# Optimization experiments

Hardware: AMD Instinct MI355X
Metric: run time of the kernel (lower is better)

The kernel has to match this reference:

```python
import jax, jax.numpy as jnp
import numpy as np

N = 100_000   # nodes
E = 1_600_000 # edges (avg degree 16)
B = 512       # graphs in batch
F_IN = 64; H = 4; D = 64; HD = H * D; EXTRA = 16
NEG_SLOPE = 0.2  # DGL GATConv default


def _gat_conv(x, src, dst, W, al, ar, bias):
    """DGL GATConv: fc -> per-head attn logits -> edge leaky_relu -> segment softmax over dst -> scatter-sum."""
    h = (x @ W).reshape(N, H, D)                       # [N,H,D]
    el = jnp.sum(h * al, axis=-1)                      # [N,H]
    er = jnp.sum(h * ar, axis=-1)                      # [N,H]
    e = jax.nn.leaky_relu(el[src] + er[dst], NEG_SLOPE)  # [E,H]
    m = jax.ops.segment_max(e, dst, num_segments=N)    # [N,H]
    m = jnp.where(jnp.isfinite(m), m, 0.0)             # guard empty segments
    ex = jnp.exp(e - m[dst])                           # [E,H]
    den = jax.ops.segment_sum(ex, dst, num_segments=N) # [N,H]
    alpha = ex / jnp.maximum(den[dst], 1e-9)           # [E,H]
    msg = h[src] * alpha[:, :, None]                   # [E,H,D]
    out = jax.ops.segment_sum(msg, dst, num_segments=N) + bias.reshape(1, H, D)
    return out  # [N,H,D]


def setup_inputs() -> dict:
    key = jax.random.key(0)
    ks = jax.random.split(key, 26)
    nrm = lambda k, shape: jax.random.normal(k, shape, dtype=jnp.float32) * 0.5
    src = jax.random.randint(ks[0], (E,), 0, N)
    # ensure every node has >=1 incoming edge (DGL disallows zero in-degree by default)
    dst = jnp.concatenate([jnp.arange(N), jax.random.randint(ks[1], (E - N,), 0, N)])
    node_graph = jnp.sort(jax.random.randint(ks[2], (N,), 0, B))
    inp = dict(
        src=src, dst=dst, node_graph=node_graph,
        feats_node=jax.random.normal(ks[3], (N, F_IN), dtype=jnp.float32),
        feats_graph=jax.random.normal(ks[4], (B, EXTRA), dtype=jnp.float32),
        W1=nrm(ks[5], (F_IN, HD)), al1=nrm(ks[6], (H, D)), ar1=nrm(ks[7], (H, D)), bg1=jnp.zeros(HD),
        W2=nrm(ks[8], (HD, HD)),  al2=nrm(ks[9], (H, D)), ar2=nrm(ks[10], (H, D)), bg2=jnp.zeros(HD),
        W3=nrm(ks[11], (HD, HD)), al3=nrm(ks[12], (H, D)), ar3=nrm(ks[13], (H, D)), bg3=jnp.zeros(HD),
        sw=nrm(ks[14], (HD, 1)), sb=jnp.zeros(1),
        lw1=nrm(ks[15], (HD + EXTRA, 2 * D)), lb1=jnp.zeros(2 * D),
        lw2=nrm(ks[16], (2 * D, D)), lb2=jnp.zeros(D),
        lw3=nrm(ks[17], (D, 1)), lb3=jnp.zeros(1),
    )
    return inp


def reference(src, dst, node_graph, feats_node, feats_graph,
              W1, al1, ar1, bg1, W2, al2, ar2, bg2, W3, al3, ar3, bg3,
              sw, sb, lw1, lb1, lw2, lb2, lw3, lb3):
    selu = jax.nn.selu
    x = selu(_gat_conv(feats_node, src, dst, W1, al1, ar1, bg1)).reshape(N, HD)
    x = selu(_gat_conv(x, src, dst, W2, al2, ar2, bg2)).reshape(N, HD)
    x = selu(_gat_conv(x, src, dst, W3, al3, ar3, bg3)).reshape(N, HD)
    # WeightedAverage readout: sigmoid-scored weighted mean per graph
    w = jax.nn.sigmoid(x @ sw + sb)                               # [N,1]
    num = jax.ops.segment_sum(w * x, node_graph, num_segments=B)  # [B,HD]
    den = jax.ops.segment_sum(w, node_graph, num_segments=B)      # [B,1]
    emb = num / jnp.maximum(den, 1e-9)
    y = jnp.concatenate([emb, feats_graph], axis=1)
    y = selu(y @ lw1 + lb1)
    y = selu(y @ lw2 + lb2)
    return y @ lw3 + lb3  # [B,1]
```

## Files before the change

kernel.cpp:

```cpp
#include <hip/hip_runtime.h>

#define N_NODES 100000
#define N_EDGES 1600000
#define N_GRAPHS 512
#define F_IN 64
#define HD 256
#define EXTRA 16
#define SCAN_BLOCK 512

typedef float f32x4 __attribute__((ext_vector_type(4)));
typedef _Float16 f16x4 __attribute__((ext_vector_type(4)));
typedef _Float16 f16x8 __attribute__((ext_vector_type(8)));

__device__ __forceinline__ float selu_f(float x) {
    const float a = 1.6732632423543772f, sc = 1.0507009873554805f;
    return x > 0.f ? sc * x : sc * a * (__expf(x) - 1.f);
}

__global__ __launch_bounds__(256) void hist_k(const int* __restrict__ dst, int* __restrict__ hist) {
    int j = blockIdx.x * 256 + threadIdx.x;
    if (j < N_EDGES) atomicAdd(&hist[dst[j]], 1);
}

__global__ __launch_bounds__(SCAN_BLOCK) void scan1_k(const int* __restrict__ hist,
                                                      int* __restrict__ row_ptr,
                                                      int* __restrict__ bsums) {
    __shared__ int sm[SCAN_BLOCK];
    int t = threadIdx.x;
    int i = blockIdx.x * SCAN_BLOCK + t;
    int v = (i < N_NODES) ? hist[i] : 0;
    sm[t] = v;
    __syncthreads();
    for (int off = 1; off < SCAN_BLOCK; off <<= 1) {
        int add = (t >= off) ? sm[t - off] : 0;
        __syncthreads();
        sm[t] += add;
        __syncthreads();
    }
    if (i < N_NODES) row_ptr[i] = sm[t] - v;
    if (t == SCAN_BLOCK - 1) bsums[blockIdx.x] = sm[t];
}

__global__ __launch_bounds__(256) void scan2_k(int* __restrict__ bsums, int nb) {
    __shared__ int sm[256];
    int t = threadIdx.x;
    int v = (t < nb) ? bsums[t] : 0;
    sm[t] = v;
    __syncthreads();
    for (int off = 1; off < 256; off <<= 1) {
        int add = (t >= off) ? sm[t - off] : 0;
        __syncthreads();
        sm[t] += add;
        __syncthreads();
    }
    if (t < nb) bsums[t] = sm[t] - v;
}

__global__ __launch_bounds__(256) void scan3_k(int* __restrict__ row_ptr, const int* __restrict__ bsums) {
    int i = blockIdx.x * 256 + threadIdx.x;
    if (i < N_NODES) row_ptr[i] += bsums[i / SCAN_BLOCK];
    if (i == 0) row_ptr[N_NODES] = N_EDGES;
}

__global__ __launch_bounds__(256) void scatter_k(const int* __restrict__ src,
                                                 const int* __restrict__ dst,
                                                 const int* __restrict__ row_ptr,
                                                 int* __restrict__ cursor,
                                                 int* __restrict__ csr_src) {
    int j = blockIdx.x * 256 + threadIdx.x;
    if (j < N_EDGES) {
        int d = dst[j];
        int r = atomicAdd(&cursor[d], 1);
        csr_src[row_ptr[d] + r] = src[j];
    }
}

__global__ __launch_bounds__(256) void gbound_k(const int* __restrict__ node_graph, int* __restrict__ gstart) {
    int g = blockIdx.x * 256 + threadIdx.x;
    if (g > N_GRAPHS) return;
    int lo = 0, hi = N_NODES;
    while (lo < hi) {
        int mid = (lo + hi) >> 1;
        if (node_graph[mid] < g) lo = mid + 1; else hi = mid;
    }
    gstart[g] = lo;
}

__global__ __launch_bounds__(256) void tcast_split_k(const float* __restrict__ W,
                                                     _Float16* __restrict__ Wt_hi,
                                                     _Float16* __restrict__ Wt_lo, int K) {
    int idx = blockIdx.x * 256 + threadIdx.x;
    if (idx >= K * HD) return;
    int n = idx / K, k = idx - n * K;
    float w = W[(size_t)k * HD + n];
    _Float16 hi = (_Float16)w;
    _Float16 lo = (_Float16)(w - (float)hi);
    Wt_hi[idx] = hi;
    Wt_lo[idx] = lo;
}

template <int K>
__global__ __launch_bounds__(256) void gemm_split_k(const float* __restrict__ A,
                                                    const _Float16* __restrict__ Bt_hi,
                                                    const _Float16* __restrict__ Bt_lo,
                                                    const float* __restrict__ al,
                                                    const float* __restrict__ ar,
                                                    _Float16* __restrict__ Chi,
                                                    float* __restrict__ el,
                                                    float* __restrict__ er, int M) {
    const int BM = 128, BN = 128, LDP = 40;
    __shared__ _Float16 As_hi[BM][LDP];
    __shared__ _Float16 As_lo[BM][LDP];
    __shared__ _Float16 Bs_hi[BN][LDP];
    __shared__ _Float16 Bs_lo[BN][LDP];
    int tid = threadIdx.x;
    int wave = tid >> 6, lane = tid & 63;
    int q = lane >> 4, l16 = lane & 15;
    int row0 = blockIdx.y * BM, col0 = blockIdx.x * BN;
    f32x4 acc[2][8] = {};

    for (int k0 = 0; k0 < K; k0 += 32) {
#pragma unroll
        for (int c = 0; c < 4; c++) {
            int cc = tid + c * 256;
            int r = cc >> 3, o = (cc & 7) * 4;
            int gr = row0 + r;
            float4 v = make_float4(0.f, 0.f, 0.f, 0.f);
            if (gr < M) v = *(const float4*)(A + (size_t)gr * K + k0 + o);
            f16x4 hi, lo;
            hi.x = (_Float16)v.x; lo.x = (_Float16)(v.x - (float)hi.x);
            hi.y = (_Float16)v.y; lo.y = (_Float16)(v.y - (float)hi.y);
            hi.z = (_Float16)v.z; lo.z = (_Float16)(v.z - (float)hi.z);
            hi.w = (_Float16)v.w; lo.w = (_Float16)(v.w - (float)hi.w);
            *(f16x4*)&As_hi[r][o] = hi;
            *(f16x4*)&As_lo[r][o] = lo;
        }
#pragma unroll
        for (int c = 0; c < 2; c++) {
            int cc = tid + c * 256;
            int n = cc >> 2, o = (cc & 3) * 8;
            *(f16x8*)&Bs_hi[n][o] = *(const f16x8*)(Bt_hi + (size_t)(col0 + n) * K + k0 + o);
            *(f16x8*)&Bs_lo[n][o] = *(const f16x8*)(Bt_lo + (size_t)(col0 + n) * K + k0 + o);
        }
        __syncthreads();

        f16x8 ah[2], alo2[2];
#pragma unroll
        for (int ms = 0; ms < 2; ms++) {
            int m = wave * 32 + ms * 16 + l16;
            ah[ms] = *(const f16x8*)&As_hi[m][q * 8];
            alo2[ms] = *(const f16x8*)&As_lo[m][q * 8];
        }
#pragma unroll
        for (int ns = 0; ns < 8; ns++) {
            int n = ns * 16 + l16;
            f16x8 bh = *(const f16x8*)&Bs_hi[n][q * 8];
            f16x8 bl = *(const f16x8*)&Bs_lo[n][q * 8];
#pragma unroll
            for (int ms = 0; ms < 2; ms++) {
                acc[ms][ns] = __builtin_amdgcn_mfma_f32_16x16x32_f16(ah[ms], bh, acc[ms][ns], 0, 0, 0);
                acc[ms][ns] = __builtin_amdgcn_mfma_f32_16x16x32_f16(ah[ms], bl, acc[ms][ns], 0, 0, 0);
                acc[ms][ns] = __builtin_amdgcn_mfma_f32_16x16x32_f16(alo2[ms], bh, acc[ms][ns], 0, 0, 0);
            }
        }
        __syncthreads();
    }

    const int h0 = col0 >> 6;
    float alv[8], arv[8];
#pragma unroll
    for (int ns = 0; ns < 8; ns++) {
        int hh = h0 + (ns >> 2);
        int d = (ns & 3) * 16 + l16;
        alv[ns] = al[hh * 64 + d];
        arv[ns] = ar[hh * 64 + d];
    }
#pragma unroll
    for (int ms = 0; ms < 2; ms++) {
#pragma unroll
        for (int i = 0; i < 4; i++) {
            int r = row0 + wave * 32 + ms * 16 + q * 4 + i;
            bool ok = r < M;
            float el0 = 0.f, er0 = 0.f, el1 = 0.f, er1 = 0.f;
#pragma unroll
            for (int ns = 0; ns < 8; ns++) {
                float v = acc[ms][ns][i];
                if (ok) Chi[(size_t)r * HD + col0 + ns * 16 + l16] = (_Float16)v;
                if (ns < 4) { el0 = fmaf(v, alv[ns], el0); er0 = fmaf(v, arv[ns], er0); }
                else        { el1 = fmaf(v, alv[ns], el1); er1 = fmaf(v, arv[ns], er1); }
            }
#pragma unroll
            for (int off = 1; off < 16; off <<= 1) {
                el0 += __shfl_xor(el0, off, 64);
                er0 += __shfl_xor(er0, off, 64);
                el1 += __shfl_xor(el1, off, 64);
                er1 += __shfl_xor(er1, off, 64);
            }
            if (l16 == 0 && ok) {
                el[(size_t)r * 4 + h0] = el0;
                el[(size_t)r * 4 + h0 + 1] = el1;
                er[(size_t)r * 4 + h0] = er0;
                er[(size_t)r * 4 + h0 + 1] = er1;
            }
        }
    }
}

__global__ __launch_bounds__(256) void gat_aggregate_k(const _Float16* __restrict__ hb,
                                                       const float* __restrict__ el,
                                                       const float* __restrict__ er,
                                                       const int* __restrict__ csr_src,
                                                       const int* __restrict__ row_ptr,
                                                       const float* __restrict__ bias,
                                                       float* __restrict__ xout) {
    __shared__ float wlds[4][64][4];
    __shared__ int snlds[4][64];
    int wv = threadIdx.x >> 6;
    int lane = threadIdx.x & 63;
    int v = blockIdx.x * 4 + wv;
    bool valid = v < N_NODES;
    int vc = valid ? v : 0;
    int rs = row_ptr[vc];
    int deg = valid ? row_ptr[vc + 1] - rs : 0;
    float4 erv = make_float4(0.f, 0.f, 0.f, 0.f);
    if (valid) erv = *(const float4*)(er + (size_t)vc * 4);

    float m[4] = {-1e30f, -1e30f, -1e30f, -1e30f};
    float s[4] = {0.f, 0.f, 0.f, 0.f};
    float m_h = 0.f, inv_den = 1.f, er_h = 0.f;
    int head = lane >> 4;

    if (deg <= 64) {
        int my_sn = 0;
        float my_e[4] = {0.f, 0.f, 0.f, 0.f};
        if (lane < deg) {
            int sn = csr_src[rs + lane];
            my_sn = sn;
            float4 elv = *(const float4*)(el + (size_t)sn * 4);
            float e0 = elv.x + erv.x, e1 = elv.y + erv.y, e2 = elv.z + erv.z, e3 = elv.w + erv.w;
            my_e[0] = e0 > 0.f ? e0 : 0.2f * e0;
            my_e[1] = e1 > 0.f ? e1 : 0.2f * e1;
            my_e[2] = e2 > 0.f ? e2 : 0.2f * e2;
            my_e[3] = e3 > 0.f ? e3 : 0.2f * e3;
#pragma unroll
            for (int hh = 0; hh < 4; hh++) { m[hh] = my_e[hh]; s[hh] = 1.f; }
        }
        for (int off = 1; off < deg && off < 64; off <<= 1) {
#pragma unroll
            for (int hh = 0; hh < 4; hh++) {
                float mo = __shfl_xor(m[hh], off, 64);
                float so = __shfl_xor(s[hh], off, 64);
                float mn = fmaxf(m[hh], mo);
                s[hh] = s[hh] * __expf(m[hh] - mn) + so * __expf(mo - mn);
                m[hh] = mn;
            }
        }
        if (lane < deg) {
#pragma unroll
            for (int hh = 0; hh < 4; hh++)
                wlds[wv][lane][hh] = __expf(my_e[hh] - m[hh]) / fmaxf(s[hh], 1e-9f);
            snlds[wv][lane] = my_sn;
        }
    } else {
        for (int t = lane; t < deg; t += 64) {
            int sn = csr_src[rs + t];
            float4 elv = *(const float4*)(el + (size_t)sn * 4);
            float e[4];
            e[0] = elv.x + erv.x; e[1] = elv.y + erv.y; e[2] = elv.z + erv.z; e[3] = elv.w + erv.w;
#pragma unroll
            for (int hh = 0; hh < 4; hh++) {
                float ev = e[hh] > 0.f ? e[hh] : 0.2f * e[hh];
                float mn = fmaxf(m[hh], ev);
                s[hh] = s[hh] * __expf(m[hh] - mn) + __expf(ev - mn);
                m[hh] = mn;
            }
        }
#pragma unroll
        for (int off = 32; off >= 1; off >>= 1) {
#pragma unroll
            for (int hh = 0; hh < 4; hh++) {
                float mo = __shfl_xor(m[hh], off, 64);
                float so = __shfl_xor(s[hh], off, 64);
                float mn = fmaxf(m[hh], mo);
                s[hh] = s[hh] * __expf(m[hh] - mn) + so * __expf(mo - mn);
                m[hh] = mn;
            }
        }
        m_h = head == 0 ? m[0] : head == 1 ? m[1] : head == 2 ? m[2] : m[3];
        float den = head == 0 ? s[0] : head == 1 ? s[1] : head == 2 ? s[2] : s[3];
        er_h = head == 0 ? erv.x : head == 1 ? erv.y : head == 2 ? erv.z : erv.w;
        inv_den = 1.f / fmaxf(den, 1e-9f);
    }
    __syncthreads();

    float a0 = 0.f, a1 = 0.f, a2 = 0.f, a3 = 0.f;
    if (deg <= 64) {
        int t = 0;
        for (; t + 8 <= deg; t += 8) {
            int sn[8];
            float w[8];
#pragma unroll
            for (int u = 0; u < 8; u++) {
                sn[u] = snlds[wv][t + u];
                w[u] = wlds[wv][t + u][head];
            }
            f16x4 hv[8];
#pragma unroll
            for (int u = 0; u < 8; u++)
                hv[u] = *(const f16x4*)(hb + (size_t)sn[u] * HD + lane * 4);
#pragma unroll
            for (int u = 0; u < 8; u++) {
                a0 = fmaf(w[u], (float)hv[u].x, a0);
                a1 = fmaf(w[u], (float)hv[u].y, a1);
                a2 = fmaf(w[u], (float)hv[u].z, a2);
                a3 = fmaf(w[u], (float)hv[u].w, a3);
            }
        }
        for (; t < deg; t++) {
            int sn = snlds[wv][t];
            float w = wlds[wv][t][head];
            f16x4 hv = *(const f16x4*)(hb + (size_t)sn * HD + lane * 4);
            a0 = fmaf(w, (float)hv.x, a0);
            a1 = fmaf(w, (float)hv.y, a1);
            a2 = fmaf(w, (float)hv.z, a2);
            a3 = fmaf(w, (float)hv.w, a3);
        }
    } else {
        for (int t = 0; t < deg; t++) {
            int sn = csr_src[rs + t];
            float e = el[(size_t)sn * 4 + head] + er_h;
            e = e > 0.f ? e : 0.2f * e;
            float w = __expf(e - m_h) * inv_den;
            f16x4 hv = *(const f16x4*)(hb + (size_t)sn * HD + lane * 4);
            a0 = fmaf(w, (float)hv.x, a0);
            a1 = fmaf(w, (float)hv.y, a1);
            a2 = fmaf(w, (float)hv.z, a2);
            a3 = fmaf(w, (float)hv.w, a3);
        }
    }
    if (valid) {
        float4 bv = *(const float4*)(bias + lane * 4);
        float4 o;
        o.x = selu_f(a0 + bv.x);
        o.y = selu_f(a1 + bv.y);
        o.z = selu_f(a2 + bv.z);
        o.w = selu_f(a3 + bv.w);
        *(float4*)(xout + (size_t)v * HD + lane * 4) = o;
    }
}

__global__ __launch_bounds__(256) void score_k(const float* __restrict__ x,
                                               const float* __restrict__ sw,
                                               const float* __restrict__ sb,
                                               float* __restrict__ wsc) {
    int n = (blockIdx.x * 256 + threadIdx.x) / 64;
    int lane = threadIdx.x & 63;
    if (n >= N_NODES) return;
    float4 xv = *(const float4*)(x + (size_t)n * HD + lane * 4);
    float4 sv = *(const float4*)(sw + lane * 4);
    float p = xv.x * sv.x + xv.y * sv.y + xv.z * sv.z + xv.w * sv.w;
#pragma unroll
    for (int off = 1; off < 64; off <<= 1) p += __shfl_xor(p, off, 64);
    if (lane == 0) wsc[n] = 1.f / (1.f + __expf(-(p + sb[0])));
}

__global__ __launch_bounds__(256) void readout_k(const float* __restrict__ x,
                                                 const float* __restrict__ wsc,
                                                 const int* __restrict__ gstart,
                                                 const float* __restrict__ fg,
                                                 float* __restrict__ y0) {
    int g = blockIdx.x;
    int f = threadIdx.x;
    int s = gstart[g], e = gstart[g + 1];
    float num = 0.f, den = 0.f;
    for (int n = s; n < e; n++) {
        float wn = wsc[n];
        num = fmaf(wn, x[(size_t)n * HD + f], num);
        den += wn;
    }
    float emb = num / fmaxf(den, 1e-9f);
    y0[(size_t)g * 272 + f] = emb;
    if (f < EXTRA) y0[(size_t)g * 272 + 256 + f] = fg[g * EXTRA + f];
}

__global__ __launch_bounds__(128) void mlp_k(const float* __restrict__ y0g,
                                             const float* __restrict__ lw1, const float* __restrict__ lb1,
                                             const float* __restrict__ lw2, const float* __restrict__ lb2,
                                             const float* __restrict__ lw3, const float* __restrict__ lb3,
                                             float* __restrict__ out) {
    __shared__ float y0s[272];
    __shared__ float y1s[128];
    int g = blockIdx.x, t = threadIdx.x;
    for (int i = t; i < 272; i += 128) y0s[i] = y0g[(size_t)g * 272 + i];
    __syncthreads();
    float acc = lb1[t];
    for (int k = 0; k < 272; k++) acc = fmaf(y0s[k], lw1[k * 128 + t], acc);
    y1s[t] = selu_f(acc);
    __syncthreads();
    if (t < 64) {
        float a2 = lb2[t];
        for (int k = 0; k < 128; k++) a2 = fmaf(y1s[k], lw2[k * 64 + t], a2);
        float v2 = selu_f(a2);
        float p = v2 * lw3[t];
#pragma unroll
        for (int off = 1; off < 64; off <<= 1) p += __shfl_xor(p, off, 64);
        if (t == 0) out[g] = p + lb3[0];
    }
}

extern "C" void kernel_launch(void* const* d_in, const int* in_sizes, int n_in,
                              void* d_out, int out_size, void* d_ws, size_t ws_size,
                              hipStream_t stream) {
    const int* src = (const int*)d_in[0];
    const int* dst = (const int*)d_in[1];
    const int* node_graph = (const int*)d_in[2];
    const float* feats_node = (const float*)d_in[3];
    const float* feats_graph = (const float*)d_in[4];
    const float* W1 = (const float*)d_in[5];
    const float* al1 = (const float*)d_in[6];
    const float* ar1 = (const float*)d_in[7];
    const float* bg1 = (const float*)d_in[8];
    const float* W2 = (const float*)d_in[9];
    const float* al2 = (const float*)d_in[10];
    const float* ar2 = (const float*)d_in[11];
    const float* bg2 = (const float*)d_in[12];
    const float* W3 = (const float*)d_in[13];
    const float* al3 = (const float*)d_in[14];
    const float* ar3 = (const float*)d_in[15];
    const float* bg3 = (const float*)d_in[16];
    const float* sw = (const float*)d_in[17];
    const float* sb = (const float*)d_in[18];
    const float* lw1 = (const float*)d_in[19];
    const float* lb1 = (const float*)d_in[20];
    const float* lw2 = (const float*)d_in[21];
    const float* lb2 = (const float*)d_in[22];
    const float* lw3 = (const float*)d_in[23];
    const float* lb3 = (const float*)d_in[24];
    float* out = (float*)d_out;

    char* ws = (char*)d_ws;
    size_t off = 0;
    auto alloc = [&](size_t bytes) -> char* {
        char* p = ws + off;
        off += (bytes + 255) & ~(size_t)255;
        return p;
    };
    float* xf32 = (float*)alloc((size_t)N_NODES * HD * 4);
    _Float16* hhi = (_Float16*)alloc((size_t)N_NODES * HD * 2);
    _Float16* W1hi = (_Float16*)alloc((size_t)F_IN * HD * 2);
    _Float16* W1lo = (_Float16*)alloc((size_t)F_IN * HD * 2);
    _Float16* W2hi = (_Float16*)alloc((size_t)HD * HD * 2);
    _Float16* W2lo = (_Float16*)alloc((size_t)HD * HD * 2);
    _Float16* W3hi = (_Float16*)alloc((size_t)HD * HD * 2);
    _Float16* W3lo = (_Float16*)alloc((size_t)HD * HD * 2);
    float* el = (float*)alloc((size_t)N_NODES * 4 * 4);
    float* er = (float*)alloc((size_t)N_NODES * 4 * 4);
    float* wsc = (float*)alloc((size_t)N_NODES * 4);
    float* y0 = (float*)alloc((size_t)N_GRAPHS * 272 * 4);
    int* hist = (int*)alloc((size_t)N_NODES * 4);
    int* row_ptr = (int*)alloc((size_t)(N_NODES + 1) * 4);
    int* cursor = (int*)alloc((size_t)N_NODES * 4);
    int* csr_src = (int*)alloc((size_t)N_EDGES * 4);
    int* gstart = (int*)alloc((size_t)(N_GRAPHS + 1) * 4);
    int* bsums = (int*)alloc(256 * 4);
    (void)ws_size; (void)in_sizes; (void)n_in; (void)out_size;

    hipMemsetAsync(hist, 0, (size_t)N_NODES * 4, stream);
    hipMemsetAsync(cursor, 0, (size_t)N_NODES * 4, stream);

    hist_k<<<(N_EDGES + 255) / 256, 256, 0, stream>>>(dst, hist);
    int nb = (N_NODES + SCAN_BLOCK - 1) / SCAN_BLOCK;
    scan1_k<<<nb, SCAN_BLOCK, 0, stream>>>(hist, row_ptr, bsums);
    scan2_k<<<1, 256, 0, stream>>>(bsums, nb);
    scan3_k<<<(N_NODES + 255) / 256, 256, 0, stream>>>(row_ptr, bsums);
    scatter_k<<<(N_EDGES + 255) / 256, 256, 0, stream>>>(src, dst, row_ptr, cursor, csr_src);
    gbound_k<<<3, 256, 0, stream>>>(node_graph, gstart);

    tcast_split_k<<<(F_IN * HD + 255) / 256, 256, 0, stream>>>(W1, W1hi, W1lo, F_IN);
    tcast_split_k<<<(HD * HD + 255) / 256, 256, 0, stream>>>(W2, W2hi, W2lo, HD);
    tcast_split_k<<<(HD * HD + 255) / 256, 256, 0, stream>>>(W3, W3hi, W3lo, HD);

    dim3 ggrid(HD / 128, (N_NODES + 127) / 128);
    int nwb = (N_NODES + 3) / 4;

    gemm_split_k<F_IN><<<ggrid, 256, 0, stream>>>(feats_node, W1hi, W1lo, al1, ar1, hhi, el, er, N_NODES);
    gat_aggregate_k<<<nwb, 256, 0, stream>>>(hhi, el, er, csr_src, row_ptr, bg1, xf32);
    gemm_split_k<HD><<<ggrid, 256, 0, stream>>>(xf32, W2hi, W2lo, al2, ar2, hhi, el, er, N_NODES);
    gat_aggregate_k<<<nwb, 256, 0, stream>>>(hhi, el, er, csr_src, row_ptr, bg2, xf32);
    gemm_split_k<HD><<<ggrid, 256, 0, stream>>>(xf32, W3hi, W3lo, al3, ar3, hhi, el, er, N_NODES);
    gat_aggregate_k<<<nwb, 256, 0, stream>>>(hhi, el, er, csr_src, row_ptr, bg3, xf32);

    score_k<<<nwb, 256, 0, stream>>>(xf32, sw, sb, wsc);
    readout_k<<<N_GRAPHS, 256, 0, stream>>>(xf32, wsc, gstart, feats_graph, y0);
    mlp_k<<<N_GRAPHS, 128, 0, stream>>>(y0, lw1, lb1, lw2, lb2, lw3, lb3, out);
}
```

Baseline: 1.012 ms.

## Fuse readout scoring into last aggregate and defer softmax normalization

The sigmoid score computation moves into the final GAT aggregation kernel via a template flag, which removes the separate score kernel and its re-read of the node feature matrix. The small-degree softmax switches from an online max/sum shuffle merge to a separate max pass followed by a sum pass. Normalization by the denominator is applied once at the output instead of per edge weight. The readout loop also gets an unroll hint. The risk is small extra register pressure in the aggregate kernel and a slightly different floating-point ordering.

```diff
diff --git a/kernel.cpp b/kernel.cpp
--- a/kernel.cpp
+++ b/kernel.cpp
@@ -206,13 +206,17 @@
     }
 }
 
+template <int OUT>
 __global__ __launch_bounds__(256) void gat_aggregate_k(const _Float16* __restrict__ hb,
                                                        const float* __restrict__ el,
                                                        const float* __restrict__ er,
                                                        const int* __restrict__ csr_src,
                                                        const int* __restrict__ row_ptr,
                                                        const float* __restrict__ bias,
-                                                       float* __restrict__ xout) {
+                                                       float* __restrict__ xout,
+                                                       const float* __restrict__ sw,
+                                                       const float* __restrict__ sb,
+                                                       float* __restrict__ wsc) {
     __shared__ float wlds[4][64][4];
     __shared__ int snlds[4][64];
     int wv = threadIdx.x >> 6;
@@ -225,43 +229,55 @@
     float4 erv = make_float4(0.f, 0.f, 0.f, 0.f);
     if (valid) erv = *(const float4*)(er + (size_t)vc * 4);
 
-    float m[4] = {-1e30f, -1e30f, -1e30f, -1e30f};
-    float s[4] = {0.f, 0.f, 0.f, 0.f};
-    float m_h = 0.f, inv_den = 1.f, er_h = 0.f;
     int head = lane >> 4;
+    float inv_den = 1.f;
+    float m_h = 0.f, er_h = 0.f;
 
     if (deg <= 64) {
+        float e0 = -1e30f, e1 = -1e30f, e2 = -1e30f, e3 = -1e30f;
         int my_sn = 0;
-        float my_e[4] = {0.f, 0.f, 0.f, 0.f};
         if (lane < deg) {
-            int sn = csr_src[rs + lane];
-            my_sn = sn;
-            float4 elv = *(const float4*)(el + (size_t)sn * 4);
-            float e0 = elv.x + erv.x, e1 = elv.y + erv.y, e2 = elv.z + erv.z, e3 = elv.w + erv.w;
-            my_e[0] = e0 > 0.f ? e0 : 0.2f * e0;
-            my_e[1] = e1 > 0.f ? e1 : 0.2f * e1;
-            my_e[2] = e2 > 0.f ? e2 : 0.2f * e2;
-            my_e[3] = e3 > 0.f ? e3 : 0.2f * e3;
-#pragma unroll
-            for (int hh = 0; hh < 4; hh++) { m[hh] = my_e[hh]; s[hh] = 1.f; }
-        }
-        for (int off = 1; off < deg && off < 64; off <<= 1) {
-#pragma unroll
-            for (int hh = 0; hh < 4; hh++) {
-                float mo = __shfl_xor(m[hh], off, 64);
-                float so = __shfl_xor(s[hh], off, 64);
-                float mn = fmaxf(m[hh], mo);
-                s[hh] = s[hh] * __expf(m[hh] - mn) + so * __expf(mo - mn);
-                m[hh] = mn;
-            }
-        }
+            my_sn = csr_src[rs + lane];
+            float4 elv = *(const float4*)(el + (size_t)my_sn * 4);
+            float t0 = elv.x + erv.x, t1 = elv.y + erv.y, t2 = elv.z + erv.z, t3 = elv.w + erv.w;
+            e0 = t0 > 0.f ? t0 : 0.2f * t0;
+            e1 = t1 > 0.f ? t1 : 0.2f * t1;
+            e2 = t2 > 0.f ? t2 : 0.2f * t2;
+            e3 = t3 > 0.f ? t3 : 0.2f * t3;
+        }
+        float m0 = e0, m1 = e1, m2 = e2, m3 = e3;
+        for (int off = 1; off < deg; off <<= 1) {
+            m0 = fmaxf(m0, __shfl_xor(m0, off, 64));
+            m1 = fmaxf(m1, __shfl_xor(m1, off, 64));
+            m2 = fmaxf(m2, __shfl_xor(m2, off, 64));
+            m3 = fmaxf(m3, __shfl_xor(m3, off, 64));
+        }
+        float p0 = 0.f, p1 = 0.f, p2 = 0.f, p3 = 0.f;
         if (lane < deg) {
-#pragma unroll
-            for (int hh = 0; hh < 4; hh++)
-                wlds[wv][lane][hh] = __expf(my_e[hh] - m[hh]) / fmaxf(s[hh], 1e-9f);
+            p0 = __expf(e0 - m0); p1 = __expf(e1 - m1);
+            p2 = __expf(e2 - m2); p3 = __expf(e3 - m3);
+        }
+        float s0 = p0, s1 = p1, s2 = p2, s3 = p3;
+        for (int off = 1; off < deg; off <<= 1) {
+            s0 += __shfl_xor(s0, off, 64);
+            s1 += __shfl_xor(s1, off, 64);
+            s2 += __shfl_xor(s2, off, 64);
+            s3 += __shfl_xor(s3, off, 64);
+        }
+        float d0 = __shfl(s0, 0, 64), d1 = __shfl(s1, 0, 64);
+        float d2 = __shfl(s2, 0, 64), d3 = __shfl(s3, 0, 64);
+        float den = head == 0 ? d0 : head == 1 ? d1 : head == 2 ? d2 : d3;
+        inv_den = 1.f / fmaxf(den, 1e-9f);
+        if (lane < deg) {
+            wlds[wv][lane][0] = p0;
+            wlds[wv][lane][1] = p1;
+            wlds[wv][lane][2] = p2;
+            wlds[wv][lane][3] = p3;
             snlds[wv][lane] = my_sn;
         }
     } else {
+        float m[4] = {-1e30f, -1e30f, -1e30f, -1e30f};
+        float s[4] = {0.f, 0.f, 0.f, 0.f};
         for (int t = lane; t < deg; t += 64) {
             int sn = csr_src[rs + t];
             float4 elv = *(const float4*)(el + (size_t)sn * 4);
@@ -330,7 +346,7 @@
             int sn = csr_src[rs + t];
             float e = el[(size_t)sn * 4 + head] + er_h;
             e = e > 0.f ? e : 0.2f * e;
-            float w = __expf(e - m_h) * inv_den;
+            float w = __expf(e - m_h);
             f16x4 hv = *(const f16x4*)(hb + (size_t)sn * HD + lane * 4);
             a0 = fmaf(w, (float)hv.x, a0);
             a1 = fmaf(w, (float)hv.y, a1);
@@ -338,30 +354,21 @@
             a3 = fmaf(w, (float)hv.w, a3);
         }
     }
-    if (valid) {
-        float4 bv = *(const float4*)(bias + lane * 4);
-        float4 o;
-        o.x = selu_f(a0 + bv.x);
-        o.y = selu_f(a1 + bv.y);
-        o.z = selu_f(a2 + bv.z);
-        o.w = selu_f(a3 + bv.w);
-        *(float4*)(xout + (size_t)v * HD + lane * 4) = o;
-    }
-}
-
-__global__ __launch_bounds__(256) void score_k(const float* __restrict__ x,
-                                               const float* __restrict__ sw,
-                                               const float* __restrict__ sb,
-                                               float* __restrict__ wsc) {
-    int n = (blockIdx.x * 256 + threadIdx.x) / 64;
-    int lane = threadIdx.x & 63;
-    if (n >= N_NODES) return;
-    float4 xv = *(const float4*)(x + (size_t)n * HD + lane * 4);
-    float4 sv = *(const float4*)(sw + lane * 4);
-    float p = xv.x * sv.x + xv.y * sv.y + xv.z * sv.z + xv.w * sv.w;
-#pragma unroll
-    for (int off = 1; off < 64; off <<= 1) p += __shfl_xor(p, off, 64);
-    if (lane == 0) wsc[n] = 1.f / (1.f + __expf(-(p + sb[0])));
+    float4 bv = *(const float4*)(bias + lane * 4);
+    float4 o;
+    o.x = selu_f(fmaf(a0, inv_den, bv.x));
+    o.y = selu_f(fmaf(a1, inv_den, bv.y));
+    o.z = selu_f(fmaf(a2, inv_den, bv.z));
+    o.w = selu_f(fmaf(a3, inv_den, bv.w));
+    if (valid) *(float4*)(xout + (size_t)v * HD + lane * 4) = o;
+
+    if constexpr (OUT == 1) {
+        float4 sv = *(const float4*)(sw + lane * 4);
+        float p = o.x * sv.x + o.y * sv.y + o.z * sv.z + o.w * sv.w;
+#pragma unroll
+        for (int off = 1; off < 64; off <<= 1) p += __shfl_xor(p, off, 64);
+        if (lane == 0 && valid) wsc[v] = 1.f / (1.f + __expf(-(p + sb[0])));
+    }
 }
 
 __global__ __launch_bounds__(256) void readout_k(const float* __restrict__ x,
@@ -373,6 +380,7 @@
     int f = threadIdx.x;
     int s = gstart[g], e = gstart[g + 1];
     float num = 0.f, den = 0.f;
+#pragma unroll 4
     for (int n = s; n < e; n++) {
         float wn = wsc[n];
         num = fmaf(wn, x[(size_t)n * HD + f], num);
@@ -484,13 +492,12 @@
     int nwb = (N_NODES + 3) / 4;
 
     gemm_split_k<F_IN><<<ggrid, 256, 0, stream>>>(feats_node, W1hi, W1lo, al1, ar1, hhi, el, er, N_NODES);
-    gat_aggregate_k<<<nwb, 256, 0, stream>>>(hhi, el, er, csr_src, row_ptr, bg1, xf32);
+    gat_aggregate_k<0><<<nwb, 256, 0, stream>>>(hhi, el, er, csr_src, row_ptr, bg1, xf32, nullptr, nullptr, nullptr);
     gemm_split_k<HD><<<ggrid, 256, 0, stream>>>(xf32, W2hi, W2lo, al2, ar2, hhi, el, er, N_NODES);
-    gat_aggregate_k<<<nwb, 256, 0, stream>>>(hhi, el, er, csr_src, row_ptr, bg2, xf32);
+    gat_aggregate_k<0><<<nwb, 256, 0, stream>>>(hhi, el, er, csr_src, row_ptr, bg2, xf32, nullptr, nullptr, nullptr);
     gemm_split_k<HD><<<ggrid, 256, 0, stream>>>(xf32, W3hi, W3lo, al3, ar3, hhi, el, er, N_NODES);
-    gat_aggregate_k<<<nwb, 256, 0, stream>>>(hhi, el, er, csr_src, row_ptr, bg3, xf32);
-
-    score_k<<<nwb, 256, 0, stream>>>(xf32, sw, sb, wsc);
+    gat_aggregate_k<1><<<nwb, 256, 0, stream>>>(hhi, el, er, csr_src, row_ptr, bg3, xf32, sw, sb, wsc);
+
     readout_k<<<N_GRAPHS, 256, 0, stream>>>(xf32, wsc, gstart, feats_graph, y0);
     mlp_k<<<N_GRAPHS, 128, 0, stream>>>(y0, lw1, lb1, lw2, lb2, lw3, lb3, out);
 }
```

Result: faster. 973.0 us (-3.8%).
